# Kernel optimization log

Measured on AMD Instinct MI355X. Metric: run time of the kernel, lower is better.

## Reference

```python
import jax, jax.numpy as jnp
import numpy as np


def _fixed_bernoulli(key, heads, rows, cols, connectivity):
    # Each column gets exactly k = max(1, int(connectivity*rows)) ones (as in _fixed_bernoulli).
    k = max(1, int(connectivity * rows))
    r = jax.random.uniform(key, (heads, rows, cols))
    thr = jnp.sort(r, axis=1)[:, k - 1:k, :]  # k-th smallest per (head, col)
    return (r <= thr).astype(jnp.float32)


def _spectral_radius(W, iters=80):
    # Power-iteration estimate of |lambda_max| per head (replaces torch.linalg.eigvals at init).
    U, N, _ = W.shape
    v0 = jnp.ones((U, N), jnp.float32) / np.sqrt(N)

    def body(v, _):
        w = jnp.einsum('unm,um->un', W, v)
        nrm = jnp.linalg.norm(w, axis=-1, keepdims=True)
        return w / nrm, nrm[:, 0]

    _, nrms = jax.lax.scan(body, v0, None, length=iters)
    return jnp.mean(nrms[-10:], axis=0)  # damp oscillation from complex eigenpairs


def setup_inputs() -> dict:
    key = jax.random.key(0)
    ks = jax.random.split(key, 10)
    B, U, N, D, O = 64, 16, 2048, 1024, 1024
    X = jax.random.normal(ks[0], (B, U, D), jnp.float32)
    state = jax.random.normal(ks[1], (B, U, N), jnp.float32)
    Wmask = _fixed_bernoulli(ks[2], U, N, N, 0.2)
    W = jax.random.normal(ks[3], (U, N, N), jnp.float32) * Wmask
    W = W / _spectral_radius(W)[:, None, None]  # W buffer is normalized to spectral radius ~1
    Win = _fixed_bernoulli(ks[4], U, D, N, 0.2)  # 0/1 fixed-bernoulli input weights
    bias = (jax.random.uniform(ks[5], (U, 1, N)) < 0.5).astype(jnp.float32)
    Wout = jax.random.normal(ks[6], (U, N, O), jnp.float32)
    adaptive_lr = jax.random.uniform(ks[7], (U, D, 1), jnp.float32)
    sr = jax.random.uniform(ks[8], (U, 1, 1), jnp.float32)
    temperature = jnp.ones((1,), jnp.float32)
    return {"X": X, "state": state, "W": W, "Win": Win, "bias": bias,
            "Wout": Wout, "adaptive_lr": adaptive_lr, "sr": sr, "temperature": temperature}


def reference(X, state, W, Win, bias, Wout, adaptive_lr, sr, temperature):
    # X: [B,U,D], state: [B,U,N]
    # lr: softmax over the units axis of (X @ adaptive_lr) / temperature -> [B,U,1]
    lr = jax.nn.softmax(jnp.einsum('bud,udk->buk', X, adaptive_lr) / temperature, axis=1)
    feed = jnp.einsum('bud,udn->bun', X, Win)
    # _sparse_mm_subhead(state, W*sr, ...) + bias == per-unit state @ (W*sr) + bias
    echo = jnp.einsum('bun,unm->bum', state, W * sr) + bias[:, 0, :]
    new_state = (1.0 - lr) * state + lr * jnp.tanh(feed + echo)  # [B,U,N]
    output = jnp.einsum('bun,uno->buo', new_state, Wout)  # [B,U,O]
    return (new_state, output)
```

## Files before the change

### kernel.cpp

```cpp
#include <hip/hip_runtime.h>
#include <hip/hip_bf16.h>
#include <stdint.h>

typedef __attribute__((ext_vector_type(8))) short short8;
typedef __attribute__((ext_vector_type(4))) float f32x4;

#define BB 64
#define UU 16
#define NN 2048
#define DD 1024
#define OO 1024

static __device__ __forceinline__ float bf2f(unsigned short v){
  union { unsigned int u; float f; } c; c.u = ((unsigned int)v) << 16; return c.f;
}
static __device__ __forceinline__ unsigned short f2bf(float f){
  union { float f; unsigned int u; } c; c.f = f;
  unsigned int u = c.u;
  unsigned int r = (u + 0x7FFFu + ((u >> 16) & 1u)) >> 16;
  return (unsigned short)r;
}
static __device__ __forceinline__ bool is_bf16_buf(const void* temp){
  return ((*(const unsigned int*)temp) & 0xFFFFu) == 0x3F80u;
}

__global__ __launch_bounds__(256)
void lr_kernel(const void* Xv, const void* alrv, const void* tempv, float* lrp)
{
  const bool isbf = is_bf16_buf(tempv);
  const int b = blockIdx.x;
  __shared__ float s[16];
  const int lane = threadIdx.x & 63;
  const int wave = threadIdx.x >> 6;
  for (int uu = 0; uu < 4; ++uu){
    const int u = wave * 4 + uu;
    float acc = 0.0f;
    if (isbf){
      const unsigned short* X = (const unsigned short*)Xv + ((size_t)(b*UU + u))*DD;
      const unsigned short* A = (const unsigned short*)alrv + (size_t)u*DD;
      for (int d = lane; d < DD; d += 64) acc += bf2f(X[d]) * bf2f(A[d]);
    } else {
      const float* X = (const float*)Xv + ((size_t)(b*UU + u))*DD;
      const float* A = (const float*)alrv + (size_t)u*DD;
      for (int d = lane; d < DD; d += 64) acc += X[d] * A[d];
    }
    #pragma unroll
    for (int off = 32; off; off >>= 1) acc += __shfl_down(acc, off, 64);
    if (lane == 0) s[u] = acc;
  }
  __syncthreads();
  if (threadIdx.x == 0){
    const float t = isbf ? bf2f(*(const unsigned short*)tempv) : *(const float*)tempv;
    float mx = -3.0e38f;
    #pragma unroll
    for (int u = 0; u < 16; ++u){ s[u] /= t; mx = fmaxf(mx, s[u]); }
    float e[16], sum = 0.0f;
    #pragma unroll
    for (int u = 0; u < 16; ++u){ e[u] = expf(s[u] - mx); sum += e[u]; }
    #pragma unroll
    for (int u = 0; u < 16; ++u) lrp[b*16 + u] = e[u] / sum;
  }
}

__global__ __launch_bounds__(256)
void ns_kernel(const void* Xv, const void* Sv, const void* Wv, const void* Winv,
               const void* biasv, const void* srv, const void* tempv,
               const float* lrp, void* outv)
{
  const bool isbf = is_bf16_buf(tempv);
  const int u   = blockIdx.y;
  const int n0  = blockIdx.x * 64;
  const int tid = threadIdx.x;
  const int lane = tid & 63;
  const int wave = tid >> 6;

  __shared__ unsigned short As[64*40];
  __shared__ unsigned short Ws[32*64];

  const int arow = tid >> 2;
  const int akk  = (tid & 3) << 3;
  const int wk   = tid >> 3;
  const int wn   = (tid & 7) << 3;

  const float srval = isbf ? bf2f(((const unsigned short*)srv)[u]) : ((const float*)srv)[u];

  f32x4 acc[4] = {};
  short8 areg, wreg;

  auto stage_load = [&](int k0){
    {
      const int kg = k0 + akk;
      const void* base; size_t off;
      if (kg < DD){ base = Xv; off = ((size_t)(arow*UU + u))*DD + kg; }
      else        { base = Sv; off = ((size_t)(arow*UU + u))*NN + (kg - DD); }
      if (isbf){
        areg = *(const short8*)((const unsigned short*)base + off);
      } else {
        const f32x4* p = (const f32x4*)((const float*)base + off);
        f32x4 a0 = p[0], a1 = p[1];
        #pragma unroll
        for (int j = 0; j < 4; ++j){ areg[j] = (short)f2bf(a0[j]); areg[4+j] = (short)f2bf(a1[j]); }
      }
    }
    {
      const int kg = k0 + wk;
      const void* base; size_t off; float sc;
      if (kg < DD){ base = Winv; off = ((size_t)(u*DD + kg))*NN + n0 + wn; sc = 1.0f; }
      else        { base = Wv;   off = ((size_t)(u*NN + (kg - DD)))*NN + n0 + wn; sc = srval; }
      if (isbf){
        short8 v = *(const short8*)((const unsigned short*)base + off);
        #pragma unroll
        for (int j = 0; j < 8; ++j) wreg[j] = (short)f2bf(bf2f((unsigned short)v[j]) * sc);
      } else {
        const f32x4* p = (const f32x4*)((const float*)base + off);
        f32x4 a0 = p[0], a1 = p[1];
        #pragma unroll
        for (int j = 0; j < 4; ++j){ wreg[j] = (short)f2bf(a0[j]*sc); wreg[4+j] = (short)f2bf(a1[j]*sc); }
      }
    }
  };

  stage_load(0);
  const int NCH = (DD + NN) / 32;
  #pragma unroll 1
  for (int c = 0; c < NCH; ++c){
    *(short8*)&As[arow*40 + akk] = areg;
    *(short8*)&Ws[wk*64 + wn]    = wreg;
    __syncthreads();
    if (c + 1 < NCH) stage_load((c + 1) * 32);

    const int colg = wave*16 + (lane & 15);
    const int q = lane >> 4;
    short8 af[4];
    #pragma unroll
    for (int mt = 0; mt < 4; ++mt)
      af[mt] = *(const short8*)&As[(mt*16 + (lane & 15))*40 + q*8];
    short8 bfv;
    #pragma unroll
    for (int j = 0; j < 8; ++j) bfv[j] = (short)Ws[(q*8 + j)*64 + colg];
    #pragma unroll
    for (int mt = 0; mt < 4; ++mt)
      acc[mt] = __builtin_amdgcn_mfma_f32_16x16x32_bf16(af[mt], bfv, acc[mt], 0, 0, 0);
    __syncthreads();
  }

  {
    const int q = lane >> 4;
    const int col = n0 + wave*16 + (lane & 15);
    const float bval = isbf ? bf2f(((const unsigned short*)biasv)[u*NN + col])
                            : ((const float*)biasv)[u*NN + col];
    #pragma unroll
    for (int mt = 0; mt < 4; ++mt){
      #pragma unroll
      for (int r = 0; r < 4; ++r){
        const int b = mt*16 + q*4 + r;
        const size_t idx = ((size_t)(b*UU + u))*NN + col;
        const float sold = isbf ? bf2f(((const unsigned short*)Sv)[idx]) : ((const float*)Sv)[idx];
        const float l = lrp[b*16 + u];
        const float tval = tanhf(acc[mt][r] + bval);
        const float ns = (1.0f - l)*sold + l*tval;
        if (isbf) ((unsigned short*)outv)[idx] = f2bf(ns);
        else      ((float*)outv)[idx] = ns;
      }
    }
  }
}

__global__ __launch_bounds__(256)
void out_kernel(const void* NSv, const void* Woutv, const void* tempv, void* outv)
{
  const bool isbf = is_bf16_buf(tempv);
  const int u   = blockIdx.y;
  const int n0  = blockIdx.x * 64;
  const int tid = threadIdx.x;
  const int lane = tid & 63;
  const int wave = tid >> 6;

  __shared__ unsigned short As[64*40];
  __shared__ unsigned short Ws[32*64];

  const int arow = tid >> 2;
  const int akk  = (tid & 3) << 3;
  const int wk   = tid >> 3;
  const int wn   = (tid & 7) << 3;

  f32x4 acc[4] = {};
  short8 areg, wreg;

  auto stage_load = [&](int k0){
    {
      const int kg = k0 + akk;
      const size_t off = ((size_t)(arow*UU + u))*NN + kg;
      if (isbf){
        areg = *(const short8*)((const unsigned short*)NSv + off);
      } else {
        const f32x4* p = (const f32x4*)((const float*)NSv + off);
        f32x4 a0 = p[0], a1 = p[1];
        #pragma unroll
        for (int j = 0; j < 4; ++j){ areg[j] = (short)f2bf(a0[j]); areg[4+j] = (short)f2bf(a1[j]); }
      }
    }
    {
      const int kg = k0 + wk;
      const size_t off = ((size_t)(u*NN + kg))*OO + n0 + wn;
      if (isbf){
        wreg = *(const short8*)((const unsigned short*)Woutv + off);
      } else {
        const f32x4* p = (const f32x4*)((const float*)Woutv + off);
        f32x4 a0 = p[0], a1 = p[1];
        #pragma unroll
        for (int j = 0; j < 4; ++j){ wreg[j] = (short)f2bf(a0[j]); wreg[4+j] = (short)f2bf(a1[j]); }
      }
    }
  };

  stage_load(0);
  const int NCH = NN / 32;
  #pragma unroll 1
  for (int c = 0; c < NCH; ++c){
    *(short8*)&As[arow*40 + akk] = areg;
    *(short8*)&Ws[wk*64 + wn]    = wreg;
    __syncthreads();
    if (c + 1 < NCH) stage_load((c + 1) * 32);

    const int colg = wave*16 + (lane & 15);
    const int q = lane >> 4;
    short8 af[4];
    #pragma unroll
    for (int mt = 0; mt < 4; ++mt)
      af[mt] = *(const short8*)&As[(mt*16 + (lane & 15))*40 + q*8];
    short8 bfv;
    #pragma unroll
    for (int j = 0; j < 8; ++j) bfv[j] = (short)Ws[(q*8 + j)*64 + colg];
    #pragma unroll
    for (int mt = 0; mt < 4; ++mt)
      acc[mt] = __builtin_amdgcn_mfma_f32_16x16x32_bf16(af[mt], bfv, acc[mt], 0, 0, 0);
    __syncthreads();
  }

  {
    const int q = lane >> 4;
    const int col = n0 + wave*16 + (lane & 15);
    #pragma unroll
    for (int mt = 0; mt < 4; ++mt){
      #pragma unroll
      for (int r = 0; r < 4; ++r){
        const int b = mt*16 + q*4 + r;
        const size_t idx = ((size_t)(b*UU + u))*OO + col;
        if (isbf) ((unsigned short*)outv)[(size_t)BB*UU*NN + idx] = f2bf(acc[mt][r]);
        else      ((float*)outv)[(size_t)BB*UU*NN + idx] = acc[mt][r];
      }
    }
  }
}

extern "C" void kernel_launch(void* const* d_in, const int* in_sizes, int n_in,
                              void* d_out, int out_size, void* d_ws, size_t ws_size,
                              hipStream_t stream)
{
  const void* X    = d_in[0];
  const void* st   = d_in[1];
  const void* W    = d_in[2];
  const void* Win  = d_in[3];
  const void* bias = d_in[4];
  const void* Wout = d_in[5];
  const void* alr  = d_in[6];
  const void* sr   = d_in[7];
  const void* temp = d_in[8];

  float* lrbuf = (float*)d_ws;

  lr_kernel<<<dim3(BB), dim3(256), 0, stream>>>(X, alr, temp, lrbuf);
  ns_kernel<<<dim3(NN/64, UU), dim3(256), 0, stream>>>(X, st, W, Win, bias, sr, temp, lrbuf, d_out);
  out_kernel<<<dim3(OO/64, UU), dim3(256), 0, stream>>>(d_out, Wout, temp, d_out);
}
```

Baseline: 671.6 us.

## Double-buffer LDS, halve N-tile per block, and hoist sr scaling to epilogue

Both GEMM kernels now use double-buffered shared memory with a two-stage register prefetch, so global loads for chunk c+2 overlap compute on chunk c and each iteration needs one barrier instead of two. The output-column tile per block shrinks from 64 to 32, doubling the grid to raise occupancy, and the four waves are arranged 2x2 over the tile. The sr scale on W is no longer applied per element during loading. Instead, separate accumulators for the feed and echo parts are combined in the epilogue as accF + sr*accE. The risks are that the smaller tile lowers reuse of the A operand, since X and state are reloaded by twice as many blocks, and the extra buffer uses more LDS.

```diff
diff --git a/kernel.cpp b/kernel.cpp
--- a/kernel.cpp
+++ b/kernel.cpp
@@ -1,8 +1,8 @@
 #include <hip/hip_runtime.h>
-#include <hip/hip_bf16.h>
 #include <stdint.h>
 
 typedef __attribute__((ext_vector_type(8))) short short8;
+typedef __attribute__((ext_vector_type(4))) short s16x4;
 typedef __attribute__((ext_vector_type(4))) float f32x4;
 
 #define BB 64
@@ -22,6 +22,13 @@
 }
 static __device__ __forceinline__ bool is_bf16_buf(const void* temp){
   return ((*(const unsigned int*)temp) & 0xFFFFu) == 0x3F80u;
+}
+static __device__ __forceinline__ short8 cvt8(const float* p){
+  f32x4 a0 = *(const f32x4*)p, a1 = *(const f32x4*)(p + 4);
+  short8 r;
+  #pragma unroll
+  for (int j = 0; j < 4; ++j){ r[j] = (short)f2bf(a0[j]); r[4+j] = (short)f2bf(a1[j]); }
+  return r;
 }
 
 __global__ __launch_bounds__(256)
@@ -69,98 +76,118 @@
 {
   const bool isbf = is_bf16_buf(tempv);
   const int u   = blockIdx.y;
-  const int n0  = blockIdx.x * 64;
+  const int n0  = blockIdx.x * 32;
   const int tid = threadIdx.x;
   const int lane = tid & 63;
   const int wave = tid >> 6;
-
-  __shared__ unsigned short As[64*40];
-  __shared__ unsigned short Ws[32*64];
+  const int wm = wave >> 1;
+  const int wn = wave & 1;
+  const int q  = lane >> 4;
+  const int m  = lane & 15;
+
+  __shared__ unsigned short As[2][64*40];
+  __shared__ unsigned short Ws[2][32*36];
+
+  const float srval = isbf ? bf2f(((const unsigned short*)srv)[u]) : ((const float*)srv)[u];
 
   const int arow = tid >> 2;
   const int akk  = (tid & 3) << 3;
-  const int wk   = tid >> 3;
-  const int wn   = (tid & 7) << 3;
-
-  const float srval = isbf ? bf2f(((const unsigned short*)srv)[u]) : ((const float*)srv)[u];
-
-  f32x4 acc[4] = {};
+  const int wk   = tid >> 2;
+  const int wn8  = (tid & 3) << 3;
+
   short8 areg, wreg;
 
   auto stage_load = [&](int k0){
     {
       const int kg = k0 + akk;
-      const void* base; size_t off;
-      if (kg < DD){ base = Xv; off = ((size_t)(arow*UU + u))*DD + kg; }
-      else        { base = Sv; off = ((size_t)(arow*UU + u))*NN + (kg - DD); }
       if (isbf){
-        areg = *(const short8*)((const unsigned short*)base + off);
+        const unsigned short* p = (kg < DD)
+          ? (const unsigned short*)Xv + ((size_t)(arow*UU + u))*DD + kg
+          : (const unsigned short*)Sv + ((size_t)(arow*UU + u))*NN + (kg - DD);
+        areg = *(const short8*)p;
       } else {
-        const f32x4* p = (const f32x4*)((const float*)base + off);
-        f32x4 a0 = p[0], a1 = p[1];
-        #pragma unroll
-        for (int j = 0; j < 4; ++j){ areg[j] = (short)f2bf(a0[j]); areg[4+j] = (short)f2bf(a1[j]); }
-      }
-    }
-    {
+        const float* p = (kg < DD)
+          ? (const float*)Xv + ((size_t)(arow*UU + u))*DD + kg
+          : (const float*)Sv + ((size_t)(arow*UU + u))*NN + (kg - DD);
+        areg = cvt8(p);
+      }
+    }
+    if (tid < 128){
       const int kg = k0 + wk;
-      const void* base; size_t off; float sc;
-      if (kg < DD){ base = Winv; off = ((size_t)(u*DD + kg))*NN + n0 + wn; sc = 1.0f; }
-      else        { base = Wv;   off = ((size_t)(u*NN + (kg - DD)))*NN + n0 + wn; sc = srval; }
       if (isbf){
-        short8 v = *(const short8*)((const unsigned short*)base + off);
-        #pragma unroll
-        for (int j = 0; j < 8; ++j) wreg[j] = (short)f2bf(bf2f((unsigned short)v[j]) * sc);
+        const unsigned short* p = (kg < DD)
+          ? (const unsigned short*)Winv + ((size_t)(u*DD + kg))*NN + n0 + wn8
+          : (const unsigned short*)Wv   + ((size_t)(u*NN + (kg - DD)))*NN + n0 + wn8;
+        wreg = *(const short8*)p;
       } else {
-        const f32x4* p = (const f32x4*)((const float*)base + off);
-        f32x4 a0 = p[0], a1 = p[1];
-        #pragma unroll
-        for (int j = 0; j < 4; ++j){ wreg[j] = (short)f2bf(a0[j]*sc); wreg[4+j] = (short)f2bf(a1[j]*sc); }
+        const float* p = (kg < DD)
+          ? (const float*)Winv + ((size_t)(u*DD + kg))*NN + n0 + wn8
+          : (const float*)Wv   + ((size_t)(u*NN + (kg - DD)))*NN + n0 + wn8;
+        wreg = cvt8(p);
       }
     }
   };
 
+  auto stage_write = [&](int buf){
+    *(short8*)&As[buf][arow*40 + akk] = areg;
+    if (tid < 128){
+      s16x4 lo, hi;
+      #pragma unroll
+      for (int j = 0; j < 4; ++j){ lo[j] = wreg[j]; hi[j] = wreg[4+j]; }
+      *(s16x4*)&Ws[buf][wk*36 + wn8]     = lo;
+      *(s16x4*)&Ws[buf][wk*36 + wn8 + 4] = hi;
+    }
+  };
+
+  f32x4 accF[2] = {};
+  f32x4 accE[2] = {};
+
+  const int NCH = (DD + NN) / 32;
   stage_load(0);
-  const int NCH = (DD + NN) / 32;
+  stage_write(0);
+  stage_load(32);
+  __syncthreads();
+
   #pragma unroll 1
   for (int c = 0; c < NCH; ++c){
-    *(short8*)&As[arow*40 + akk] = areg;
-    *(short8*)&Ws[wk*64 + wn]    = wreg;
+    const int buf = c & 1;
+    if (c + 1 < NCH) stage_write(buf ^ 1);
+    if (c + 2 < NCH) stage_load((c + 2) * 32);
+
+    const int colg = wn*16 + m;
+    short8 af0 = *(const short8*)&As[buf][(wm*32 +  0 + m)*40 + q*8];
+    short8 af1 = *(const short8*)&As[buf][(wm*32 + 16 + m)*40 + q*8];
+    short8 bfv;
+    #pragma unroll
+    for (int j = 0; j < 8; ++j) bfv[j] = (short)Ws[buf][(q*8 + j)*36 + colg];
+
+    if (c < DD/32){
+      accF[0] = __builtin_amdgcn_mfma_f32_16x16x32_bf16(af0, bfv, accF[0], 0, 0, 0);
+      accF[1] = __builtin_amdgcn_mfma_f32_16x16x32_bf16(af1, bfv, accF[1], 0, 0, 0);
+    } else {
+      accE[0] = __builtin_amdgcn_mfma_f32_16x16x32_bf16(af0, bfv, accE[0], 0, 0, 0);
+      accE[1] = __builtin_amdgcn_mfma_f32_16x16x32_bf16(af1, bfv, accE[1], 0, 0, 0);
+    }
     __syncthreads();
-    if (c + 1 < NCH) stage_load((c + 1) * 32);
-
-    const int colg = wave*16 + (lane & 15);
-    const int q = lane >> 4;
-    short8 af[4];
-    #pragma unroll
-    for (int mt = 0; mt < 4; ++mt)
-      af[mt] = *(const short8*)&As[(mt*16 + (lane & 15))*40 + q*8];
-    short8 bfv;
-    #pragma unroll
-    for (int j = 0; j < 8; ++j) bfv[j] = (short)Ws[(q*8 + j)*64 + colg];
-    #pragma unroll
-    for (int mt = 0; mt < 4; ++mt)
-      acc[mt] = __builtin_amdgcn_mfma_f32_16x16x32_bf16(af[mt], bfv, acc[mt], 0, 0, 0);
-    __syncthreads();
   }
 
   {
-    const int q = lane >> 4;
-    const int col = n0 + wave*16 + (lane & 15);
+    const int col = n0 + wn*16 + m;
     const float bval = isbf ? bf2f(((const unsigned short*)biasv)[u*NN + col])
                             : ((const float*)biasv)[u*NN + col];
     #pragma unroll
-    for (int mt = 0; mt < 4; ++mt){
+    for (int mt = 0; mt < 2; ++mt){
       #pragma unroll
       for (int r = 0; r < 4; ++r){
-        const int b = mt*16 + q*4 + r;
+        const int b = wm*32 + mt*16 + q*4 + r;
         const size_t idx = ((size_t)(b*UU + u))*NN + col;
+        const float l = lrp[b*UU + u];
         const float sold = isbf ? bf2f(((const unsigned short*)Sv)[idx]) : ((const float*)Sv)[idx];
-        const float l = lrp[b*16 + u];
-        const float tval = tanhf(acc[mt][r] + bval);
-        const float ns = (1.0f - l)*sold + l*tval;
-        if (isbf) ((unsigned short*)outv)[idx] = f2bf(ns);
-        else      ((float*)outv)[idx] = ns;
+        const float val = accF[mt][r] + srval*accE[mt][r] + bval;
+        const float tv = tanhf(val);
+        const float nsv = (1.0f - l)*sold + l*tv;
+        if (isbf) ((unsigned short*)outv)[idx] = f2bf(nsv);
+        else      ((float*)outv)[idx] = nsv;
       }
     }
   }
@@ -171,81 +198,88 @@
 {
   const bool isbf = is_bf16_buf(tempv);
   const int u   = blockIdx.y;
-  const int n0  = blockIdx.x * 64;
+  const int n0  = blockIdx.x * 32;
   const int tid = threadIdx.x;
   const int lane = tid & 63;
   const int wave = tid >> 6;
-
-  __shared__ unsigned short As[64*40];
-  __shared__ unsigned short Ws[32*64];
+  const int wm = wave >> 1;
+  const int wn = wave & 1;
+  const int q  = lane >> 4;
+  const int m  = lane & 15;
+
+  __shared__ unsigned short As[2][64*40];
+  __shared__ unsigned short Ws[2][32*36];
 
   const int arow = tid >> 2;
   const int akk  = (tid & 3) << 3;
-  const int wk   = tid >> 3;
-  const int wn   = (tid & 7) << 3;
-
-  f32x4 acc[4] = {};
+  const int wk   = tid >> 2;
+  const int wn8  = (tid & 3) << 3;
+
   short8 areg, wreg;
 
   auto stage_load = [&](int k0){
     {
       const int kg = k0 + akk;
-      const size_t off = ((size_t)(arow*UU + u))*NN + kg;
       if (isbf){
-        areg = *(const short8*)((const unsigned short*)NSv + off);
+        areg = *(const short8*)((const unsigned short*)NSv + ((size_t)(arow*UU + u))*NN + kg);
       } else {
-        const f32x4* p = (const f32x4*)((const float*)NSv + off);
-        f32x4 a0 = p[0], a1 = p[1];
-        #pragma unroll
-        for (int j = 0; j < 4; ++j){ areg[j] = (short)f2bf(a0[j]); areg[4+j] = (short)f2bf(a1[j]); }
-      }
-    }
-    {
+        areg = cvt8((const float*)NSv + ((size_t)(arow*UU + u))*NN + kg);
+      }
+    }
+    if (tid < 128){
       const int kg = k0 + wk;
-      const size_t off = ((size_t)(u*NN + kg))*OO + n0 + wn;
       if (isbf){
-        wreg = *(const short8*)((const unsigned short*)Woutv + off);
+        wreg = *(const short8*)((const unsigned short*)Woutv + ((size_t)(u*NN + kg))*OO + n0 + wn8);
       } else {
-        const f32x4* p = (const f32x4*)((const float*)Woutv + off);
-        f32x4 a0 = p[0], a1 = p[1];
-        #pragma unroll
-        for (int j = 0; j < 4; ++j){ wreg[j] = (short)f2bf(a0[j]); wreg[4+j] = (short)f2bf(a1[j]); }
+        wreg = cvt8((const float*)Woutv + ((size_t)(u*NN + kg))*OO + n0 + wn8);
       }
     }
   };
 
+  auto stage_write = [&](int buf){
+    *(short8*)&As[buf][arow*40 + akk] = areg;
+    if (tid < 128){
+      s16x4 lo, hi;
+      #pragma unroll
+      for (int j = 0; j < 4; ++j){ lo[j] = wreg[j]; hi[j] = wreg[4+j]; }
+      *(s16x4*)&Ws[buf][wk*36 + wn8]     = lo;
+      *(s16x4*)&Ws[buf][wk*36 + wn8 + 4] = hi;
+    }
+  };
+
+  f32x4 acc[2] = {};
+
+  const int NCH = NN / 32;
   stage_load(0);
-  const int NCH = NN / 32;
+  stage_write(0);
+  stage_load(32);
+  __syncthreads();
+
   #pragma unroll 1
   for (int c = 0; c < NCH; ++c){
-    *(short8*)&As[arow*40 + akk] = areg;
-    *(short8*)&Ws[wk*64 + wn]    = wreg;
+    const int buf = c & 1;
+    if (c + 1 < NCH) stage_write(buf ^ 1);
+    if (c + 2 < NCH) stage_load((c + 2) * 32);
+
+    const int colg = wn*16 + m;
+    short8 af0 = *(const short8*)&As[buf][(wm*32 +  0 + m)*40 + q*8];
+    short8 af1 = *(const short8*)&As[buf][(wm*32 + 16 + m)*40 + q*8];
+    short8 bfv;
+    #pragma unroll
+    for (int j = 0; j < 8; ++j) bfv[j] = (short)Ws[buf][(q*8 + j)*36 + colg];
+
+    acc[0] = __builtin_amdgcn_mfma_f32_16x16x32_bf16(af0, bfv, acc[0], 0, 0, 0);
+    acc[1] = __builtin_amdgcn_mfma_f32_16x16x32_bf16(af1, bfv, acc[1], 0, 0, 0);
     __syncthreads();
-    if (c + 1 < NCH) stage_load((c + 1) * 32);
-
-    const int colg = wave*16 + (lane & 15);
-    const int q = lane >> 4;
-    short8 af[4];
-    #pragma unroll
-    for (int mt = 0; mt < 4; ++mt)
-      af[mt] = *(const short8*)&As[(mt*16 + (lane & 15))*40 + q*8];
-    short8 bfv;
-    #pragma unroll
-    for (int j = 0; j < 8; ++j) bfv[j] = (short)Ws[(q*8 + j)*64 + colg];
-    #pragma unroll
-    for (int mt = 0; mt < 4; ++mt)
-      acc[mt] = __builtin_amdgcn_mfma_f32_16x16x32_bf16(af[mt], bfv, acc[mt], 0, 0, 0);
-    __syncthreads();
   }
 
   {
-    const int q = lane >> 4;
-    const int col = n0 + wave*16 + (lane & 15);
-    #pragma unroll
-    for (int mt = 0; mt < 4; ++mt){
+    const int col = n0 + wn*16 + m;
+    #pragma unroll
+    for (int mt = 0; mt < 2; ++mt){
       #pragma unroll
       for (int r = 0; r < 4; ++r){
-        const int b = mt*16 + q*4 + r;
+        const int b = wm*32 + mt*16 + q*4 + r;
         const size_t idx = ((size_t)(b*UU + u))*OO + col;
         if (isbf) ((unsigned short*)outv)[(size_t)BB*UU*NN + idx] = f2bf(acc[mt][r]);
         else      ((float*)outv)[(size_t)BB*UU*NN + idx] = acc[mt][r];
@@ -271,6 +305,6 @@
   float* lrbuf = (float*)d_ws;
 
   lr_kernel<<<dim3(BB), dim3(256), 0, stream>>>(X, alr, temp, lrbuf);
-  ns_kernel<<<dim3(NN/64, UU), dim3(256), 0, stream>>>(X, st, W, Win, bias, sr, temp, lrbuf, d_out);
-  out_kernel<<<dim3(OO/64, UU), dim3(256), 0, stream>>>(d_out, Wout, temp, d_out);
-}
+  ns_kernel<<<dim3(NN/32, UU), dim3(256), 0, stream>>>(X, st, W, Win, bias, sr, temp, lrbuf, d_out);
+  out_kernel<<<dim3(OO/32, UU), dim3(256), 0, stream>>>(d_out, Wout, temp, d_out);
+}
```

Result: no change. 684.8 us (+2.0%).

## Drop LDS staging; load MFMA fragments directly from global with 3-deep register pipeline

Applied to the files above, without the earlier changes.

Both GEMM kernels stop staging tiles through shared memory with two barriers per chunk. Each lane now loads its A and B MFMA fragments straight from global memory into a triple-buffered register pipeline. The ns kernel keeps separate feed and echo accumulators and applies the sr scale once in the epilogue, instead of rescaling and re-rounding every W element. The out kernel is retiled to 32-column blocks with a 2x2 wave layout, doubling the grid. The trade-off is strided, uncoalesced per-element B loads (8 rows with 2- or 4-byte accesses per lane), more register pressure, and duplicated global reads across waves in place of LDS reuse.

```diff
diff --git a/kernel.cpp b/kernel.cpp
--- a/kernel.cpp
+++ b/kernel.cpp
@@ -1,5 +1,4 @@
 #include <hip/hip_runtime.h>
-#include <hip/hip_bf16.h>
 #include <stdint.h>
 
 typedef __attribute__((ext_vector_type(8))) short short8;
@@ -23,6 +22,15 @@
 static __device__ __forceinline__ bool is_bf16_buf(const void* temp){
   return ((*(const unsigned int*)temp) & 0xFFFFu) == 0x3F80u;
 }
+static __device__ __forceinline__ short8 cvt8(const float* p){
+  f32x4 a0 = *(const f32x4*)p, a1 = *(const f32x4*)(p + 4);
+  short8 r;
+  #pragma unroll
+  for (int j = 0; j < 4; ++j){ r[j] = (short)f2bf(a0[j]); r[4+j] = (short)f2bf(a1[j]); }
+  return r;
+}
+
+union BPack { unsigned int u[4]; short8 s; };
 
 __global__ __launch_bounds__(256)
 void lr_kernel(const void* Xv, const void* alrv, const void* tempv, float* lrp)
@@ -68,85 +76,97 @@
                const float* lrp, void* outv)
 {
   const bool isbf = is_bf16_buf(tempv);
-  const int u   = blockIdx.y;
-  const int n0  = blockIdx.x * 64;
-  const int tid = threadIdx.x;
-  const int lane = tid & 63;
-  const int wave = tid >> 6;
-
-  __shared__ unsigned short As[64*40];
-  __shared__ unsigned short Ws[32*64];
-
-  const int arow = tid >> 2;
-  const int akk  = (tid & 3) << 3;
-  const int wk   = tid >> 3;
-  const int wn   = (tid & 7) << 3;
+  const int u    = blockIdx.y;
+  const int n0   = blockIdx.x * 64;
+  const int lane = threadIdx.x & 63;
+  const int wave = threadIdx.x >> 6;
+  const int q    = lane >> 4;
+  const int m    = lane & 15;
+  const int col  = n0 + wave*16 + m;
 
   const float srval = isbf ? bf2f(((const unsigned short*)srv)[u]) : ((const float*)srv)[u];
 
-  f32x4 acc[4] = {};
-  short8 areg, wreg;
-
-  auto stage_load = [&](int k0){
-    {
-      const int kg = k0 + akk;
-      const void* base; size_t off;
-      if (kg < DD){ base = Xv; off = ((size_t)(arow*UU + u))*DD + kg; }
-      else        { base = Sv; off = ((size_t)(arow*UU + u))*NN + (kg - DD); }
-      if (isbf){
-        areg = *(const short8*)((const unsigned short*)base + off);
-      } else {
-        const f32x4* p = (const f32x4*)((const float*)base + off);
-        f32x4 a0 = p[0], a1 = p[1];
-        #pragma unroll
-        for (int j = 0; j < 4; ++j){ areg[j] = (short)f2bf(a0[j]); areg[4+j] = (short)f2bf(a1[j]); }
-      }
-    }
-    {
-      const int kg = k0 + wk;
-      const void* base; size_t off; float sc;
-      if (kg < DD){ base = Winv; off = ((size_t)(u*DD + kg))*NN + n0 + wn; sc = 1.0f; }
-      else        { base = Wv;   off = ((size_t)(u*NN + (kg - DD)))*NN + n0 + wn; sc = srval; }
-      if (isbf){
-        short8 v = *(const short8*)((const unsigned short*)base + off);
-        #pragma unroll
-        for (int j = 0; j < 8; ++j) wreg[j] = (short)f2bf(bf2f((unsigned short)v[j]) * sc);
-      } else {
-        const f32x4* p = (const f32x4*)((const float*)base + off);
-        f32x4 a0 = p[0], a1 = p[1];
-        #pragma unroll
-        for (int j = 0; j < 4; ++j){ wreg[j] = (short)f2bf(a0[j]*sc); wreg[4+j] = (short)f2bf(a1[j]*sc); }
-      }
-    }
-  };
-
-  stage_load(0);
+  int arow[4];
+  #pragma unroll
+  for (int mt = 0; mt < 4; ++mt) arow[mt] = (mt*16 + m)*UU + u;
+
+  const unsigned short* Xp = (const unsigned short*)Xv;
+  const unsigned short* Sp = (const unsigned short*)Sv;
+  const float* Xf = (const float*)Xv;
+  const float* Sf = (const float*)Sv;
+  const unsigned short* Winp = (const unsigned short*)Winv + (size_t)u*DD*NN;
+  const unsigned short* Wp   = (const unsigned short*)Wv   + (size_t)u*NN*NN;
+  const float* Winf = (const float*)Winv + (size_t)u*DD*NN;
+  const float* Wvf  = (const float*)Wv   + (size_t)u*NN*NN;
+
+  short8 A0[4], A1[4], A2[4];
+  unsigned int B0[8], B1[8], B2[8];
+
+  auto loadA = [&](short8* A, int c){
+    const int kk = c*32 + q*8;
+    if (isbf){
+      #pragma unroll
+      for (int mt = 0; mt < 4; ++mt)
+        A[mt] = (kk < DD) ? *(const short8*)(Xp + (size_t)arow[mt]*DD + kk)
+                          : *(const short8*)(Sp + (size_t)arow[mt]*NN + (kk - DD));
+    } else {
+      #pragma unroll
+      for (int mt = 0; mt < 4; ++mt)
+        A[mt] = (kk < DD) ? cvt8(Xf + (size_t)arow[mt]*DD + kk)
+                          : cvt8(Sf + (size_t)arow[mt]*NN + (kk - DD));
+    }
+  };
+  auto loadB = [&](unsigned int* B, int c){
+    const int kk = c*32 + q*8;
+    if (isbf){
+      const unsigned short* p = (kk < DD) ? Winp + (size_t)kk*NN + col
+                                          : Wp   + (size_t)(kk - DD)*NN + col;
+      #pragma unroll
+      for (int j = 0; j < 8; ++j) B[j] = p[(size_t)j*NN];
+    } else {
+      const float* p = (kk < DD) ? Winf + (size_t)kk*NN + col
+                                 : Wvf  + (size_t)(kk - DD)*NN + col;
+      #pragma unroll
+      for (int j = 0; j < 8; ++j) B[j] = f2bf(p[(size_t)j*NN]);
+    }
+  };
+
+  f32x4 accF[4] = {};
+  f32x4 accE[4] = {};
+
+  auto step = [&](short8* A, unsigned int* B, bool feed){
+    BPack bb;
+    bb.u[0] = B[0] | (B[1] << 16);
+    bb.u[1] = B[2] | (B[3] << 16);
+    bb.u[2] = B[4] | (B[5] << 16);
+    bb.u[3] = B[6] | (B[7] << 16);
+    if (feed){
+      #pragma unroll
+      for (int mt = 0; mt < 4; ++mt)
+        accF[mt] = __builtin_amdgcn_mfma_f32_16x16x32_bf16(A[mt], bb.s, accF[mt], 0, 0, 0);
+    } else {
+      #pragma unroll
+      for (int mt = 0; mt < 4; ++mt)
+        accE[mt] = __builtin_amdgcn_mfma_f32_16x16x32_bf16(A[mt], bb.s, accE[mt], 0, 0, 0);
+    }
+  };
+
   const int NCH = (DD + NN) / 32;
+  loadA(A0, 0); loadB(B0, 0);
+  loadA(A1, 1); loadB(B1, 1);
+  loadA(A2, 2); loadB(B2, 2);
+
   #pragma unroll 1
-  for (int c = 0; c < NCH; ++c){
-    *(short8*)&As[arow*40 + akk] = areg;
-    *(short8*)&Ws[wk*64 + wn]    = wreg;
-    __syncthreads();
-    if (c + 1 < NCH) stage_load((c + 1) * 32);
-
-    const int colg = wave*16 + (lane & 15);
-    const int q = lane >> 4;
-    short8 af[4];
-    #pragma unroll
-    for (int mt = 0; mt < 4; ++mt)
-      af[mt] = *(const short8*)&As[(mt*16 + (lane & 15))*40 + q*8];
-    short8 bfv;
-    #pragma unroll
-    for (int j = 0; j < 8; ++j) bfv[j] = (short)Ws[(q*8 + j)*64 + colg];
-    #pragma unroll
-    for (int mt = 0; mt < 4; ++mt)
-      acc[mt] = __builtin_amdgcn_mfma_f32_16x16x32_bf16(af[mt], bfv, acc[mt], 0, 0, 0);
-    __syncthreads();
+  for (int c = 0; c < NCH; c += 3){
+    step(A0, B0, c < 32);
+    if (c + 3 < NCH){ loadA(A0, c + 3); loadB(B0, c + 3); }
+    step(A1, B1, c + 1 < 32);
+    if (c + 4 < NCH){ loadA(A1, c + 4); loadB(B1, c + 4); }
+    step(A2, B2, c + 2 < 32);
+    if (c + 5 < NCH){ loadA(A2, c + 5); loadB(B2, c + 5); }
   }
 
   {
-    const int q = lane >> 4;
-    const int col = n0 + wave*16 + (lane & 15);
     const float bval = isbf ? bf2f(((const unsigned short*)biasv)[u*NN + col])
                             : ((const float*)biasv)[u*NN + col];
     #pragma unroll
@@ -155,12 +175,13 @@
       for (int r = 0; r < 4; ++r){
         const int b = mt*16 + q*4 + r;
         const size_t idx = ((size_t)(b*UU + u))*NN + col;
+        const float l = lrp[b*UU + u];
         const float sold = isbf ? bf2f(((const unsigned short*)Sv)[idx]) : ((const float*)Sv)[idx];
-        const float l = lrp[b*16 + u];
-        const float tval = tanhf(acc[mt][r] + bval);
-        const float ns = (1.0f - l)*sold + l*tval;
-        if (isbf) ((unsigned short*)outv)[idx] = f2bf(ns);
-        else      ((float*)outv)[idx] = ns;
+        const float val = accF[mt][r] + srval*accE[mt][r] + bval;
+        const float tv = tanhf(val);
+        const float nsv = (1.0f - l)*sold + l*tv;
+        if (isbf) ((unsigned short*)outv)[idx] = f2bf(nsv);
+        else      ((float*)outv)[idx] = nsv;
       }
     }
   }
@@ -170,82 +191,91 @@
 void out_kernel(const void* NSv, const void* Woutv, const void* tempv, void* outv)
 {
   const bool isbf = is_bf16_buf(tempv);
-  const int u   = blockIdx.y;
-  const int n0  = blockIdx.x * 64;
-  const int tid = threadIdx.x;
-  const int lane = tid & 63;
-  const int wave = tid >> 6;
-
-  __shared__ unsigned short As[64*40];
-  __shared__ unsigned short Ws[32*64];
-
-  const int arow = tid >> 2;
-  const int akk  = (tid & 3) << 3;
-  const int wk   = tid >> 3;
-  const int wn   = (tid & 7) << 3;
-
-  f32x4 acc[4] = {};
-  short8 areg, wreg;
-
-  auto stage_load = [&](int k0){
-    {
-      const int kg = k0 + akk;
-      const size_t off = ((size_t)(arow*UU + u))*NN + kg;
-      if (isbf){
-        areg = *(const short8*)((const unsigned short*)NSv + off);
-      } else {
-        const f32x4* p = (const f32x4*)((const float*)NSv + off);
-        f32x4 a0 = p[0], a1 = p[1];
-        #pragma unroll
-        for (int j = 0; j < 4; ++j){ areg[j] = (short)f2bf(a0[j]); areg[4+j] = (short)f2bf(a1[j]); }
-      }
-    }
-    {
-      const int kg = k0 + wk;
-      const size_t off = ((size_t)(u*NN + kg))*OO + n0 + wn;
-      if (isbf){
-        wreg = *(const short8*)((const unsigned short*)Woutv + off);
-      } else {
-        const f32x4* p = (const f32x4*)((const float*)Woutv + off);
-        f32x4 a0 = p[0], a1 = p[1];
-        #pragma unroll
-        for (int j = 0; j < 4; ++j){ wreg[j] = (short)f2bf(a0[j]); wreg[4+j] = (short)f2bf(a1[j]); }
-      }
-    }
-  };
-
-  stage_load(0);
+  const int u    = blockIdx.y;
+  const int n0   = blockIdx.x * 32;
+  const int lane = threadIdx.x & 63;
+  const int wave = threadIdx.x >> 6;
+  const int wc   = wave & 1;
+  const int wr   = wave >> 1;
+  const int q    = lane >> 4;
+  const int m    = lane & 15;
+  const int col  = n0 + wc*16 + m;
+
+  int arow[2];
+  #pragma unroll
+  for (int mt = 0; mt < 2; ++mt) arow[mt] = (wr*32 + mt*16 + m)*UU + u;
+
+  const unsigned short* Ap = (const unsigned short*)NSv;
+  const float* Af = (const float*)NSv;
+  const unsigned short* Wo = (const unsigned short*)Woutv + (size_t)u*NN*OO;
+  const float* Wof = (const float*)Woutv + (size_t)u*NN*OO;
+
+  short8 A0[2], A1[2], A2[2];
+  unsigned int B0[8], B1[8], B2[8];
+
+  auto loadA = [&](short8* A, int c){
+    const int kk = c*32 + q*8;
+    if (isbf){
+      #pragma unroll
+      for (int mt = 0; mt < 2; ++mt)
+        A[mt] = *(const short8*)(Ap + (size_t)arow[mt]*NN + kk);
+    } else {
+      #pragma unroll
+      for (int mt = 0; mt < 2; ++mt)
+        A[mt] = cvt8(Af + (size_t)arow[mt]*NN + kk);
+    }
+  };
+  auto loadB = [&](unsigned int* B, int c){
+    const int kk = c*32 + q*8;
+    if (isbf){
+      const unsigned short* p = Wo + (size_t)kk*OO + col;
+      #pragma unroll
+      for (int j = 0; j < 8; ++j) B[j] = p[(size_t)j*OO];
+    } else {
+      const float* p = Wof + (size_t)kk*OO + col;
+      #pragma unroll
+      for (int j = 0; j < 8; ++j) B[j] = f2bf(p[(size_t)j*OO]);
+    }
+  };
+
+  f32x4 acc[2] = {};
+
+  auto step = [&](short8* A, unsigned int* B){
+    BPack bb;
+    bb.u[0] = B[0] | (B[1] << 16);
+    bb.u[1] = B[2] | (B[3] << 16);
+    bb.u[2] = B[4] | (B[5] << 16);
+    bb.u[3] = B[6] | (B[7] << 16);
+    #pragma unroll
+    for (int mt = 0; mt < 2; ++mt)
+      acc[mt] = __builtin_amdgcn_mfma_f32_16x16x32_bf16(A[mt], bb.s, acc[mt], 0, 0, 0);
+  };
+
   const int NCH = NN / 32;
+  loadA(A0, 0); loadB(B0, 0);
+  loadA(A1, 1); loadB(B1, 1);
+  loadA(A2, 2); loadB(B2, 2);
+
   #pragma unroll 1
-  for (int c = 0; c < NCH; ++c){
-    *(short8*)&As[arow*40 + akk] = areg;
-    *(short8*)&Ws[wk*64 + wn]    = wreg;
-    __syncthreads();
-    if (c + 1 < NCH) stage_load((c + 1) * 32);
-
-    const int colg = wave*16 + (lane & 15);
-    const int q = lane >> 4;
-    short8 af[4];
-    #pragma unroll
-    for (int mt = 0; mt < 4; ++mt)
-      af[mt] = *(const short8*)&As[(mt*16 + (lane & 15))*40 + q*8];
-    short8 bfv;
-    #pragma unroll
-    for (int j = 0; j < 8; ++j) bfv[j] = (short)Ws[(q*8 + j)*64 + colg];
-    #pragma unroll
-    for (int mt = 0; mt < 4; ++mt)
-      acc[mt] = __builtin_amdgcn_mfma_f32_16x16x32_bf16(af[mt], bfv, acc[mt], 0, 0, 0);
-    __syncthreads();
+  for (int c = 0; c < NCH; c += 3){
+    step(A0, B0);
+    if (c + 3 < NCH){ loadA(A0, c + 3); loadB(B0, c + 3); }
+    if (c + 1 < NCH){
+      step(A1, B1);
+      if (c + 4 < NCH){ loadA(A1, c + 4); loadB(B1, c + 4); }
+    }
+    if (c + 2 < NCH){
+      step(A2, B2);
+      if (c + 5 < NCH){ loadA(A2, c + 5); loadB(B2, c + 5); }
+    }
   }
 
   {
-    const int q = lane >> 4;
-    const int col = n0 + wave*16 + (lane & 15);
-    #pragma unroll
-    for (int mt = 0; mt < 4; ++mt){
+    #pragma unroll
+    for (int mt = 0; mt < 2; ++mt){
       #pragma unroll
       for (int r = 0; r < 4; ++r){
-        const int b = mt*16 + q*4 + r;
+        const int b = wr*32 + mt*16 + q*4 + r;
         const size_t idx = ((size_t)(b*UU + u))*OO + col;
         if (isbf) ((unsigned short*)outv)[(size_t)BB*UU*NN + idx] = f2bf(acc[mt][r]);
         else      ((float*)outv)[(size_t)BB*UU*NN + idx] = acc[mt][r];
@@ -272,5 +302,5 @@
 
   lr_kernel<<<dim3(BB), dim3(256), 0, stream>>>(X, alr, temp, lrbuf);
   ns_kernel<<<dim3(NN/64, UU), dim3(256), 0, stream>>>(X, st, W, Win, bias, sr, temp, lrbuf, d_out);
-  out_kernel<<<dim3(OO/64, UU), dim3(256), 0, stream>>>(d_out, Wout, temp, d_out);
-}
+  out_kernel<<<dim3(OO/32, UU), dim3(256), 0, stream>>>(d_out, Wout, temp, d_out);
+}
```

Result: slower. 803.6 us (+19.7%).
